# Performance work log

Hardware: AMD Instinct MI355X
Metric: run time of the kernel (lower is better)

The kernel has to match this reference:

```python
import jax, jax.numpy as jnp
import numpy as np

CH = 64

def _maxpool2x2(x):
    # x: [B, C, H, W] -> [B, C, H//2, W//2]
    B, C, H, W = x.shape
    return x.reshape(B, C, H // 2, 2, W // 2, 2).max(axis=(3, 5))

def _conv1x1(x, w):
    # x: [B, Cin, H, W], w: [Cout, Cin] (1x1 conv, no bias)
    return jnp.einsum('oc,bchw->bohw', w, x)

def setup_inputs() -> dict:
    key = jax.random.key(0)
    ks = jax.random.split(key, 6)
    B, H, W = 4, 128, 128
    x = jax.random.normal(ks[0], (B, CH, H, W), dtype=jnp.float32)
    # spectral-norm wrapped 1x1 conv weights; SN just rescales the weight,
    # so we materialize the (already-normalized) weight matrices directly.
    w_theta = jax.random.normal(ks[1], (CH // 8, CH), dtype=jnp.float32) * 0.05
    w_phi = jax.random.normal(ks[2], (CH // 8, CH), dtype=jnp.float32) * 0.05
    w_g = jax.random.normal(ks[3], (CH // 2, CH), dtype=jnp.float32) * 0.05
    w_o = jax.random.normal(ks[4], (CH, CH // 2), dtype=jnp.float32) * 0.05
    gamma = jnp.float32(0.5)  # nonzero so attention path contributes
    return {"x": x, "w_theta": w_theta, "w_phi": w_phi, "w_g": w_g, "w_o": w_o, "gamma": gamma}

def reference(x, w_theta, w_phi, w_g, w_o, gamma):
    B, C, H, W = x.shape
    N = H * W            # query positions
    M = (H // 2) * (W // 2)  # key/value positions after 2x2 maxpool
    theta = _conv1x1(x, w_theta).reshape(B, C // 8, N)          # [B, C/8, N]
    phi = _maxpool2x2(_conv1x1(x, w_phi)).reshape(B, C // 8, M)  # [B, C/8, M]
    g = _maxpool2x2(_conv1x1(x, w_g)).reshape(B, C // 2, M)      # [B, C/2, M]
    # beta: [B, N, M] attention over pooled key positions
    scores = jnp.einsum('bcn,bcm->bnm', theta, phi)
    beta = jax.nn.softmax(scores, axis=-1)
    # o_mid: [B, C/2, N]
    o_mid = jnp.einsum('bcm,bnm->bcn', g, beta).reshape(B, C // 2, H, W)
    o = _conv1x1(o_mid, w_o)
    return gamma * o + x
```

## Files before the change

kernel.cpp:

```cpp
#include <hip/hip_runtime.h>

typedef unsigned int uint;
typedef unsigned short ushort;
typedef __attribute__((ext_vector_type(8))) short bf16x8;
typedef __attribute__((ext_vector_type(16))) float f32x16;
typedef __attribute__((ext_vector_type(4))) uint uint4v;

constexpr int BB = 4, CHN = 64, HH = 128, WW = 128;
constexpr int NN = HH * WW;
constexpr int MM = (HH / 2) * (WW / 2);
constexpr float LOG2E = 1.44269504089f;

constexpr size_t PHI_OFF = (size_t)BB * NN * 8;
constexpr size_t GT_OFF  = PHI_OFF + (size_t)BB * MM * 8;

__device__ __forceinline__ void async16(void* lds_base, const void* gsrc) {
    __builtin_amdgcn_global_load_lds(
        (const __attribute__((address_space(1))) unsigned int*)gsrc,
        (__attribute__((address_space(3))) unsigned int*)lds_base,
        16, 0, 0);
}

__device__ __forceinline__ ushort bf16r(float f) {
    uint u = __float_as_uint(f);
    u += 0x7fff + ((u >> 16) & 1);
    return (ushort)(u >> 16);
}

__device__ __forceinline__ uint pack2(float lo, float hi) {
    return (uint)bf16r(lo) | ((uint)bf16r(hi) << 16);
}

__device__ __forceinline__ bf16x8 pack8(const float* v) {
    union { uint4v u; bf16x8 x; } cv;
    cv.u = (uint4v){pack2(v[0], v[1]), pack2(v[2], v[3]),
                    pack2(v[4], v[5]), pack2(v[6], v[7])};
    return cv.x;
}

__global__ __launch_bounds__(64)
void prep_kernel(const float* __restrict__ x,
                 const float* __restrict__ w_theta,
                 const float* __restrict__ w_phi,
                 const float* __restrict__ w_g,
                 ushort* __restrict__ theta_t,
                 ushort* __restrict__ phi_b,
                 ushort* __restrict__ gTg) {
    __shared__ float wlds[48][64];
    const int lane = threadIdx.x;
    float* wl = &wlds[0][0];
    for (int i = lane; i < 512; i += 64)  wl[i] = w_theta[i] * LOG2E;
    for (int i = lane; i < 512; i += 64)  wl[512 + i] = w_phi[i];
    for (int i = lane; i < 2048; i += 64) wl[1024 + i] = w_g[i];
    __syncthreads();

    const int bid = blockIdx.x;
    const int b = bid >> 8, tile = bid & 255;
    const int rp = tile >> 2, cb = tile & 3;
    const int h2 = lane >> 5, w2 = lane & 31;
    const int n = (2 * rp + h2) * WW + 32 * cb + w2;
    const float* xb = x + (size_t)b * CHN * NN + n;

    float acc[48];
#pragma unroll
    for (int k = 0; k < 48; ++k) acc[k] = 0.f;
#pragma unroll 4
    for (int c = 0; c < CHN; ++c) {
        const float xv = xb[(size_t)c * NN];
#pragma unroll
        for (int k = 0; k < 48; ++k) acc[k] = fmaf(wlds[k][c], xv, acc[k]);
    }

    {
        uint4v tv = (uint4v){pack2(acc[0], acc[1]), pack2(acc[2], acc[3]),
                             pack2(acc[4], acc[5]), pack2(acc[6], acc[7])};
        *(uint4v*)(theta_t + ((size_t)b * NN + n) * 8) = tv;
    }

#pragma unroll
    for (int k = 8; k < 48; ++k) {
        float v = acc[k];
        v = fmaxf(v, __shfl_xor(v, 1));
        v = fmaxf(v, __shfl_xor(v, 32));
        acc[k] = v;
    }
    const int m = rp * 64 + 16 * cb + (w2 >> 1);

    if (h2 == 0 && (w2 & 1) == 0) {
        uint4v pv = (uint4v){pack2(acc[8], acc[9]),   pack2(acc[10], acc[11]),
                             pack2(acc[12], acc[13]), pack2(acc[14], acc[15])};
        *(uint4v*)(phi_b + ((size_t)b * MM + m) * 8) = pv;
    }
    const int qidx = h2 * 2 + (w2 & 1);
    ushort* gb = gTg + (((size_t)b * (MM / 8) + (m >> 3)) * 32) * 8 + (m & 7);
#pragma unroll
    for (int j = 0; j < 8; ++j) {
        const int c = qidx * 8 + j;
        gb[(size_t)c * 8] = bf16r(acc[16 + c]);
    }
}

__global__ __launch_bounds__(256)
void attn_mfma(const float* __restrict__ x,
               const ushort* __restrict__ theta_t,
               const ushort* __restrict__ phi_b,
               const ushort* __restrict__ gTg,
               const float* __restrict__ w_o,
               const float* __restrict__ gamma_p,
               float* __restrict__ out) {
    __shared__ __align__(16) ushort phiL[2][1024];
    __shared__ __align__(16) ushort gL[2][4096];
    __shared__ __align__(16) ushort P_lds[4][32][40];

    const int tid = threadIdx.x;
    const int wv = tid >> 6, ln = tid & 63;
    const int lq = ln & 31, h = ln >> 5;
    const int b = blockIdx.x >> 7;
    const int qt = blockIdx.x & 127;
    const int q0 = qt * 128 + wv * 32;

    union { uint4v u; bf16x8 v; } thc;
    thc.u = *(const uint4v*)(theta_t + ((size_t)b * NN + q0 + lq) * 8);
    const bf16x8 thB = thc.v;

    const char* phiGb = (const char*)(phi_b + (size_t)b * MM * 8);
    const char* gGb   = (const char*)(gTg + (size_t)b * MM * 32);

    f32x16 oacc, z16;
#pragma unroll
    for (int r = 0; r < 16; ++r) { oacc[r] = 0.f; z16[r] = 0.f; }
    float ssum = 0.f;

    auto stage = [&](int t, int buf) {
        for (int p = wv; p < 10; p += 4) {
            if (p < 2)
                async16(&phiL[buf][p * 512],
                        phiGb + (size_t)t * 2048 + p * 1024 + ln * 16);
            else
                async16(&gL[buf][(p - 2) * 512],
                        gGb + (size_t)t * 8192 + (p - 2) * 1024 + ln * 16);
        }
    };

    stage(0, 0);
    __syncthreads();

    for (int t = 0; t < MM / 128; ++t) {
        const int buf = t & 1;
        if (t < MM / 128 - 1) stage(t + 1, buf ^ 1);
        const ushort* pL = phiL[buf];
        const ushort* gg = gL[buf];
#pragma unroll
        for (int s = 0; s < 4; ++s) {
            bf16x8 aphi = {};
            if (h == 0) aphi = *(const bf16x8*)(pL + (s * 32 + lq) * 8);
            f32x16 S = __builtin_amdgcn_mfma_f32_32x32x16_bf16(aphi, thB, z16, 0, 0, 0);
            float e[16];
#pragma unroll
            for (int r = 0; r < 16; ++r) {
                e[r] = exp2f(fminf(S[r], 60.f));
                ssum += e[r];
            }
#pragma unroll
            for (int r = 0; r < 16; r += 2) {
                const int key = (r & 3) + 8 * (r >> 2) + 4 * h;
                *(uint*)&P_lds[wv][lq][key] = pack2(e[r], e[r + 1]);
            }
            const bf16x8 B0 = *(const bf16x8*)&P_lds[wv][lq][8 * h];
            const bf16x8 B1 = *(const bf16x8*)&P_lds[wv][lq][16 + 8 * h];
            const bf16x8 g0 = *(const bf16x8*)(gg + ((s * 4 + h) * 256 + lq * 8));
            const bf16x8 g1 = *(const bf16x8*)(gg + ((s * 4 + 2 + h) * 256 + lq * 8));
            oacc = __builtin_amdgcn_mfma_f32_32x32x16_bf16(g0, B0, oacc, 0, 0, 0);
            oacc = __builtin_amdgcn_mfma_f32_32x32x16_bf16(g1, B1, oacc, 0, 0, 0);
        }
        __syncthreads();
    }

    ssum += __shfl_xor(ssum, 32);
    const float sc = gamma_p[0] / fmaxf(ssum, 1e-30f);
    float o16[16];
#pragma unroll
    for (int r = 0; r < 16; ++r) o16[r] = oacc[r] * sc;
#pragma unroll
    for (int r = 0; r < 16; r += 2) {
        const int key = (r & 3) + 8 * (r >> 2) + 4 * h;
        *(uint*)&P_lds[wv][lq][key] = pack2(o16[r], o16[r + 1]);
    }
    const bf16x8 OB0 = *(const bf16x8*)&P_lds[wv][lq][8 * h];
    const bf16x8 OB1 = *(const bf16x8*)&P_lds[wv][lq][16 + 8 * h];

    const float* x_b = x + (size_t)b * CHN * NN;
    float* out_b = out + (size_t)b * CHN * NN;
#pragma unroll
    for (int T = 0; T < 2; ++T) {
        const int row = T * 32 + lq;
        const float* wr = w_o + row * 32;
        float wa[8], wb[8];
#pragma unroll
        for (int j = 0; j < 8; ++j) { wa[j] = wr[8 * h + j]; wb[j] = wr[16 + 8 * h + j]; }
        const bf16x8 A0 = pack8(wa);
        const bf16x8 A1 = pack8(wb);
        f32x16 C2 = __builtin_amdgcn_mfma_f32_32x32x16_bf16(A0, OB0, z16, 0, 0, 0);
        C2 = __builtin_amdgcn_mfma_f32_32x32x16_bf16(A1, OB1, C2, 0, 0, 0);
#pragma unroll
        for (int r = 0; r < 16; ++r) {
            const int oc = T * 32 + (r & 3) + 8 * (r >> 2) + 4 * h;
            const size_t idx = (size_t)oc * NN + q0 + lq;
            out_b[idx] = C2[r] + x_b[idx];
        }
    }
}

extern "C" void kernel_launch(void* const* d_in, const int* in_sizes, int n_in,
                              void* d_out, int out_size, void* d_ws, size_t ws_size,
                              hipStream_t stream) {
    const float* x       = (const float*)d_in[0];
    const float* w_theta = (const float*)d_in[1];
    const float* w_phi   = (const float*)d_in[2];
    const float* w_g     = (const float*)d_in[3];
    const float* w_o     = (const float*)d_in[4];
    const float* gamma   = (const float*)d_in[5];
    float* out = (float*)d_out;

    ushort* theta_t = (ushort*)d_ws;
    ushort* phi_b   = theta_t + PHI_OFF;
    ushort* gTg     = theta_t + GT_OFF;

    prep_kernel<<<dim3(BB * 256), dim3(64), 0, stream>>>(
        x, w_theta, w_phi, w_g, theta_t, phi_b, gTg);

    attn_mfma<<<dim3(BB * NN / 128), dim3(256), 0, stream>>>(
        x, theta_t, phi_b, gTg, w_o, gamma, out);
}
```

Measured before the change: 224.4 us.

## Split key range across waves, split prep by output, replace LDS P transpose with shuffles

The attention kernel now gives each block 64 queries and splits the key/value range in half between wave pairs, then merges the partial accumulators and softmax sums through LDS. Block count doubles and each wave walks half the keys. The P and output-operand layout conversion now uses cross-lane shuffles instead of LDS round trips, and each wave does one of the two output-channel tiles in the epilogue. The prep kernel is split into two block groups (theta/phi and g), which lowers per-thread register use but reads x twice. A launch-bounds occupancy hint is also added.

```diff
diff --git a/kernel.cpp b/kernel.cpp
--- a/kernel.cpp
+++ b/kernel.cpp
@@ -46,12 +46,16 @@
                  ushort* __restrict__ theta_t,
                  ushort* __restrict__ phi_b,
                  ushort* __restrict__ gTg) {
-    __shared__ float wlds[48][64];
+    __shared__ float wlds[32][64];
     const int lane = threadIdx.x;
+    const int part = blockIdx.y;
     float* wl = &wlds[0][0];
-    for (int i = lane; i < 512; i += 64)  wl[i] = w_theta[i] * LOG2E;
-    for (int i = lane; i < 512; i += 64)  wl[512 + i] = w_phi[i];
-    for (int i = lane; i < 2048; i += 64) wl[1024 + i] = w_g[i];
+    if (part == 0) {
+        for (int i = lane; i < 512; i += 64) wl[i] = w_theta[i] * LOG2E;
+        for (int i = lane; i < 512; i += 64) wl[512 + i] = w_phi[i];
+    } else {
+        for (int i = lane; i < 2048; i += 64) wl[i] = w_g[i];
+    }
     __syncthreads();
 
     const int bid = blockIdx.x;
@@ -60,47 +64,61 @@
     const int h2 = lane >> 5, w2 = lane & 31;
     const int n = (2 * rp + h2) * WW + 32 * cb + w2;
     const float* xb = x + (size_t)b * CHN * NN + n;
-
-    float acc[48];
-#pragma unroll
-    for (int k = 0; k < 48; ++k) acc[k] = 0.f;
+    const int m = rp * 64 + 16 * cb + (w2 >> 1);
+
+    if (part == 0) {
+        float acc[16];
+#pragma unroll
+        for (int k = 0; k < 16; ++k) acc[k] = 0.f;
 #pragma unroll 4
-    for (int c = 0; c < CHN; ++c) {
-        const float xv = xb[(size_t)c * NN];
-#pragma unroll
-        for (int k = 0; k < 48; ++k) acc[k] = fmaf(wlds[k][c], xv, acc[k]);
-    }
-
-    {
+        for (int c = 0; c < CHN; ++c) {
+            const float xv = xb[(size_t)c * NN];
+#pragma unroll
+            for (int k = 0; k < 16; ++k) acc[k] = fmaf(wlds[k][c], xv, acc[k]);
+        }
         uint4v tv = (uint4v){pack2(acc[0], acc[1]), pack2(acc[2], acc[3]),
                              pack2(acc[4], acc[5]), pack2(acc[6], acc[7])};
         *(uint4v*)(theta_t + ((size_t)b * NN + n) * 8) = tv;
-    }
-
-#pragma unroll
-    for (int k = 8; k < 48; ++k) {
-        float v = acc[k];
-        v = fmaxf(v, __shfl_xor(v, 1));
-        v = fmaxf(v, __shfl_xor(v, 32));
-        acc[k] = v;
-    }
-    const int m = rp * 64 + 16 * cb + (w2 >> 1);
-
-    if (h2 == 0 && (w2 & 1) == 0) {
-        uint4v pv = (uint4v){pack2(acc[8], acc[9]),   pack2(acc[10], acc[11]),
-                             pack2(acc[12], acc[13]), pack2(acc[14], acc[15])};
-        *(uint4v*)(phi_b + ((size_t)b * MM + m) * 8) = pv;
-    }
-    const int qidx = h2 * 2 + (w2 & 1);
-    ushort* gb = gTg + (((size_t)b * (MM / 8) + (m >> 3)) * 32) * 8 + (m & 7);
-#pragma unroll
-    for (int j = 0; j < 8; ++j) {
-        const int c = qidx * 8 + j;
-        gb[(size_t)c * 8] = bf16r(acc[16 + c]);
-    }
-}
-
-__global__ __launch_bounds__(256)
+#pragma unroll
+        for (int k = 8; k < 16; ++k) {
+            float v = acc[k];
+            v = fmaxf(v, __shfl_xor(v, 1));
+            v = fmaxf(v, __shfl_xor(v, 32));
+            acc[k] = v;
+        }
+        if (h2 == 0 && (w2 & 1) == 0) {
+            uint4v pv = (uint4v){pack2(acc[8], acc[9]),   pack2(acc[10], acc[11]),
+                                 pack2(acc[12], acc[13]), pack2(acc[14], acc[15])};
+            *(uint4v*)(phi_b + ((size_t)b * MM + m) * 8) = pv;
+        }
+    } else {
+        float acc[32];
+#pragma unroll
+        for (int k = 0; k < 32; ++k) acc[k] = 0.f;
+#pragma unroll 4
+        for (int c = 0; c < CHN; ++c) {
+            const float xv = xb[(size_t)c * NN];
+#pragma unroll
+            for (int k = 0; k < 32; ++k) acc[k] = fmaf(wlds[k][c], xv, acc[k]);
+        }
+#pragma unroll
+        for (int k = 0; k < 32; ++k) {
+            float v = acc[k];
+            v = fmaxf(v, __shfl_xor(v, 1));
+            v = fmaxf(v, __shfl_xor(v, 32));
+            acc[k] = v;
+        }
+        const int qidx = h2 * 2 + (w2 & 1);
+        ushort* gb = gTg + (((size_t)b * (MM / 8) + (m >> 3)) * 32) * 8 + (m & 7);
+#pragma unroll
+        for (int j = 0; j < 8; ++j) {
+            const int c = qidx * 8 + j;
+            gb[(size_t)c * 8] = bf16r(acc[c]);
+        }
+    }
+}
+
+__global__ __launch_bounds__(256, 4)
 void attn_mfma(const float* __restrict__ x,
                const ushort* __restrict__ theta_t,
                const ushort* __restrict__ phi_b,
@@ -108,16 +126,16 @@
                const float* __restrict__ w_o,
                const float* __restrict__ gamma_p,
                float* __restrict__ out) {
-    __shared__ __align__(16) ushort phiL[2][1024];
-    __shared__ __align__(16) ushort gL[2][4096];
-    __shared__ __align__(16) ushort P_lds[4][32][40];
+    __shared__ __align__(16) ushort phiL[2][2][1024];
+    __shared__ __align__(16) ushort gL[2][2][4096];
 
     const int tid = threadIdx.x;
     const int wv = tid >> 6, ln = tid & 63;
     const int lq = ln & 31, h = ln >> 5;
-    const int b = blockIdx.x >> 7;
-    const int qt = blockIdx.x & 127;
-    const int q0 = qt * 128 + wv * 32;
+    const int ks = wv & 1, qi = wv >> 1;
+    const int b = blockIdx.x >> 8;
+    const int qt = blockIdx.x & 255;
+    const int q0 = qt * 64 + qi * 32;
 
     union { uint4v u; bf16x8 v; } thc;
     thc.u = *(const uint4v*)(theta_t + ((size_t)b * NN + q0 + lq) * 8);
@@ -132,24 +150,25 @@
     float ssum = 0.f;
 
     auto stage = [&](int t, int buf) {
-        for (int p = wv; p < 10; p += 4) {
-            if (p < 2)
-                async16(&phiL[buf][p * 512],
-                        phiGb + (size_t)t * 2048 + p * 1024 + ln * 16);
+        for (int p = wv; p < 20; p += 4) {
+            const int half = p / 10, pp = p % 10;
+            if (pp < 2)
+                async16(&phiL[buf][half][pp * 512],
+                        phiGb + (size_t)half * 32768 + (size_t)t * 2048 + pp * 1024 + ln * 16);
             else
-                async16(&gL[buf][(p - 2) * 512],
-                        gGb + (size_t)t * 8192 + (p - 2) * 1024 + ln * 16);
+                async16(&gL[buf][half][(pp - 2) * 512],
+                        gGb + (size_t)half * 131072 + (size_t)t * 8192 + (pp - 2) * 1024 + ln * 16);
         }
     };
 
     stage(0, 0);
     __syncthreads();
 
-    for (int t = 0; t < MM / 128; ++t) {
+    for (int t = 0; t < 16; ++t) {
         const int buf = t & 1;
-        if (t < MM / 128 - 1) stage(t + 1, buf ^ 1);
-        const ushort* pL = phiL[buf];
-        const ushort* gg = gL[buf];
+        if (t < 15) stage(t + 1, buf ^ 1);
+        const ushort* pL = phiL[buf][ks];
+        const ushort* gg = gL[buf][ks];
 #pragma unroll
         for (int s = 0; s < 4; ++s) {
             bf16x8 aphi = {};
@@ -161,53 +180,68 @@
                 e[r] = exp2f(fminf(S[r], 60.f));
                 ssum += e[r];
             }
-#pragma unroll
-            for (int r = 0; r < 16; r += 2) {
-                const int key = (r & 3) + 8 * (r >> 2) + 4 * h;
-                *(uint*)&P_lds[wv][lq][key] = pack2(e[r], e[r + 1]);
-            }
-            const bf16x8 B0 = *(const bf16x8*)&P_lds[wv][lq][8 * h];
-            const bf16x8 B1 = *(const bf16x8*)&P_lds[wv][lq][16 + 8 * h];
+            uint P[8], sx[8];
+#pragma unroll
+            for (int i = 0; i < 8; ++i) P[i] = pack2(e[2 * i], e[2 * i + 1]);
+#pragma unroll
+            for (int i = 0; i < 8; ++i) sx[i] = (uint)__shfl_xor((int)P[i], 32);
+            union { uint4v u; bf16x8 v; } B0c, B1c;
+            B0c.u = (uint4v){h ? sx[2] : P[0], h ? sx[3] : P[1],
+                             h ? P[2] : sx[0], h ? P[3] : sx[1]};
+            B1c.u = (uint4v){h ? sx[6] : P[4], h ? sx[7] : P[5],
+                             h ? P[6] : sx[4], h ? P[7] : sx[5]};
             const bf16x8 g0 = *(const bf16x8*)(gg + ((s * 4 + h) * 256 + lq * 8));
             const bf16x8 g1 = *(const bf16x8*)(gg + ((s * 4 + 2 + h) * 256 + lq * 8));
-            oacc = __builtin_amdgcn_mfma_f32_32x32x16_bf16(g0, B0, oacc, 0, 0, 0);
-            oacc = __builtin_amdgcn_mfma_f32_32x32x16_bf16(g1, B1, oacc, 0, 0, 0);
+            oacc = __builtin_amdgcn_mfma_f32_32x32x16_bf16(g0, B0c.v, oacc, 0, 0, 0);
+            oacc = __builtin_amdgcn_mfma_f32_32x32x16_bf16(g1, B1c.v, oacc, 0, 0, 0);
         }
         __syncthreads();
     }
 
     ssum += __shfl_xor(ssum, 32);
+    float* comb = (float*)&gL[0][0][0];
+    const int my = ((ks * 2 + qi) * 64 + ln) * 20;
+#pragma unroll
+    for (int r = 0; r < 16; ++r) comb[my + r] = oacc[r];
+    comb[my + 16] = ssum;
+    __syncthreads();
+    const int ot = (((ks ^ 1) * 2 + qi) * 64 + ln) * 20;
+#pragma unroll
+    for (int r = 0; r < 16; ++r) oacc[r] += comb[ot + r];
+    ssum += comb[ot + 16];
+
     const float sc = gamma_p[0] / fmaxf(ssum, 1e-30f);
     float o16[16];
 #pragma unroll
     for (int r = 0; r < 16; ++r) o16[r] = oacc[r] * sc;
-#pragma unroll
-    for (int r = 0; r < 16; r += 2) {
-        const int key = (r & 3) + 8 * (r >> 2) + 4 * h;
-        *(uint*)&P_lds[wv][lq][key] = pack2(o16[r], o16[r + 1]);
-    }
-    const bf16x8 OB0 = *(const bf16x8*)&P_lds[wv][lq][8 * h];
-    const bf16x8 OB1 = *(const bf16x8*)&P_lds[wv][lq][16 + 8 * h];
+    uint OP[8], osx[8];
+#pragma unroll
+    for (int i = 0; i < 8; ++i) OP[i] = pack2(o16[2 * i], o16[2 * i + 1]);
+#pragma unroll
+    for (int i = 0; i < 8; ++i) osx[i] = (uint)__shfl_xor((int)OP[i], 32);
+    union { uint4v u; bf16x8 v; } OB0c, OB1c;
+    OB0c.u = (uint4v){h ? osx[2] : OP[0], h ? osx[3] : OP[1],
+                      h ? OP[2] : osx[0], h ? OP[3] : osx[1]};
+    OB1c.u = (uint4v){h ? osx[6] : OP[4], h ? osx[7] : OP[5],
+                      h ? OP[6] : osx[4], h ? OP[7] : osx[5]};
 
     const float* x_b = x + (size_t)b * CHN * NN;
     float* out_b = out + (size_t)b * CHN * NN;
-#pragma unroll
-    for (int T = 0; T < 2; ++T) {
-        const int row = T * 32 + lq;
-        const float* wr = w_o + row * 32;
-        float wa[8], wb[8];
-#pragma unroll
-        for (int j = 0; j < 8; ++j) { wa[j] = wr[8 * h + j]; wb[j] = wr[16 + 8 * h + j]; }
-        const bf16x8 A0 = pack8(wa);
-        const bf16x8 A1 = pack8(wb);
-        f32x16 C2 = __builtin_amdgcn_mfma_f32_32x32x16_bf16(A0, OB0, z16, 0, 0, 0);
-        C2 = __builtin_amdgcn_mfma_f32_32x32x16_bf16(A1, OB1, C2, 0, 0, 0);
-#pragma unroll
-        for (int r = 0; r < 16; ++r) {
-            const int oc = T * 32 + (r & 3) + 8 * (r >> 2) + 4 * h;
-            const size_t idx = (size_t)oc * NN + q0 + lq;
-            out_b[idx] = C2[r] + x_b[idx];
-        }
+    const int T = ks;
+    const int row = T * 32 + lq;
+    const float* wr = w_o + row * 32;
+    float wa[8], wb[8];
+#pragma unroll
+    for (int j = 0; j < 8; ++j) { wa[j] = wr[8 * h + j]; wb[j] = wr[16 + 8 * h + j]; }
+    const bf16x8 A0 = pack8(wa);
+    const bf16x8 A1 = pack8(wb);
+    f32x16 C2 = __builtin_amdgcn_mfma_f32_32x32x16_bf16(A0, OB0c.v, z16, 0, 0, 0);
+    C2 = __builtin_amdgcn_mfma_f32_32x32x16_bf16(A1, OB1c.v, C2, 0, 0, 0);
+#pragma unroll
+    for (int r = 0; r < 16; ++r) {
+        const int oc = T * 32 + (r & 3) + 8 * (r >> 2) + 4 * h;
+        const size_t idx = (size_t)oc * NN + q0 + lq;
+        out_b[idx] = C2[r] + x_b[idx];
     }
 }
 
@@ -226,9 +260,9 @@
     ushort* phi_b   = theta_t + PHI_OFF;
     ushort* gTg     = theta_t + GT_OFF;
 
-    prep_kernel<<<dim3(BB * 256), dim3(64), 0, stream>>>(
+    prep_kernel<<<dim3(BB * 256, 2), dim3(64), 0, stream>>>(
         x, w_theta, w_phi, w_g, theta_t, phi_b, gTg);
 
-    attn_mfma<<<dim3(BB * NN / 128), dim3(256), 0, stream>>>(
+    attn_mfma<<<dim3(BB * NN / 64), dim3(256), 0, stream>>>(
         x, theta_t, phi_b, gTg, w_o, gamma, out);
 }
```

New measurement: 217.1 us. 1.03x faster.
